# Kernel optimization log

Measured on AMD Instinct MI355X. Metric: run time of the kernel, lower is better.

Reference implementation:

```python
import jax, jax.numpy as jnp
import numpy as np

B, N, C = 16, 2048, 512
NUM_HEADS = 8
D = C // NUM_HEADS  # 64


def setup_inputs() -> dict:
    key = jax.random.key(0)
    ks = jax.random.split(key, 8)
    s = 0.02
    return {
        "x": jax.random.normal(ks[0], (B, N, C), dtype=jnp.float32),
        "Wq": jax.random.normal(ks[1], (D, C), dtype=jnp.float32) * s,
        "bq": jax.random.normal(ks[2], (D,), dtype=jnp.float32) * s,
        "Wk": jax.random.normal(ks[3], (D, C), dtype=jnp.float32) * s,
        "bk": jax.random.normal(ks[4], (D,), dtype=jnp.float32) * s,
        "Wv": jax.random.normal(ks[5], (C, C), dtype=jnp.float32) * s,
        "bv": jax.random.normal(ks[6], (C,), dtype=jnp.float32) * s,
        "gamma": jax.random.normal(ks[7], (1,), dtype=jnp.float32) * 0.1,
    }


def reference(x, Wq, bq, Wk, bk, Wv, bv, gamma):
    # x: [B, N, C]; torch code permutes to [B, C, N] (channels for Conv1d)
    xt = jnp.transpose(x, (0, 2, 1))                      # [B, C, N]
    # 1x1 Conv1d == pointwise linear over channel dim
    q = jnp.einsum('dc,bcn->bdn', Wq, xt) + bq[None, :, None]   # [B, D, N]
    k = jnp.einsum('dc,bcn->bdn', Wk, xt) + bk[None, :, None]   # [B, D, N]
    v = jnp.einsum('oc,bcn->bon', Wv, xt) + bv[None, :, None]   # [B, C, N]
    # energy[b, n, m] = <q[:, n], k[:, m]>
    energy = jnp.einsum('bdn,bdm->bnm', q, k)             # [B, N, N]
    attention = jax.nn.softmax(energy, axis=-1)           # [B, N, N]
    # out = bmm(v, attention^T): out[b, c, n] = sum_m v[b, c, m] * attn[b, n, m]
    out = jnp.einsum('bcm,bnm->bcn', v, attention)        # [B, C, N]
    out = gamma[0] * out + xt
    return jnp.transpose(out, (0, 2, 1))                  # [B, N, C]
```

## Files before the change

### kernel.cpp

```cpp
#include <hip/hip_runtime.h>
#include <hip/hip_bf16.h>

typedef __bf16 bf16x8 __attribute__((ext_vector_type(8)));
typedef float f32x4 __attribute__((ext_vector_type(4)));

#define B_ 16
#define N_ 2048
#define C_ 512
#define D_ 64

__device__ __forceinline__ float bf2f(ushort u) {
    union { uint i; float f; } w; w.i = ((uint)u) << 16; return w.f;
}
__device__ __forceinline__ ushort f2bf(float f) {
    union { float f; uint i; } w; w.f = f;
    uint u = w.i;
    u = (u + 0x7fffu + ((u >> 16) & 1u)) >> 16;
    return (ushort)u;
}
__device__ __forceinline__ __bf16 u2b(ushort u) {
    union { ushort s; __bf16 b; } w; w.s = u; return w.b;
}
__device__ __forceinline__ bf16x8 ld8u(const ushort* p) { return *(const bf16x8*)p; }
__device__ __forceinline__ bf16x8 ld8f(const float* p) {
    f32x4 a = *(const f32x4*)p;
    f32x4 b = *(const f32x4*)(p + 4);
    bf16x8 r;
    r[0] = u2b(f2bf(a[0])); r[1] = u2b(f2bf(a[1]));
    r[2] = u2b(f2bf(a[2])); r[3] = u2b(f2bf(a[3]));
    r[4] = u2b(f2bf(b[0])); r[5] = u2b(f2bf(b[1]));
    r[6] = u2b(f2bf(b[2])); r[7] = u2b(f2bf(b[3]));
    return r;
}

__device__ __forceinline__ void gload16(const ushort* g, ushort* l) {
    __builtin_amdgcn_global_load_lds(
        (const __attribute__((address_space(1))) void*)g,
        (__attribute__((address_space(3))) void*)l, 16, 0, 0);
}

__global__ void probe_kernel(const void* x, int* flag) {
    int lane = threadIdx.x & 63;
    ushort u = ((const ushort*)x)[lane * 2];
    float v = fabsf(bf2f(u));
    bool sane = (v > 9.3e-10f) && (v < 1.1e9f) && (v == v);
    unsigned long long m = __ballot(sane);
    if (threadIdx.x == 0) *flag = (__popcll(m) >= 48) ? 0 : 1;
}

__launch_bounds__(256, 2)
__global__ void proj_qk_kernel(const void* __restrict__ X,
                               const void* __restrict__ Wq_,
                               const void* __restrict__ bq_,
                               const void* __restrict__ Wk_,
                               const void* __restrict__ bk_,
                               ushort* __restrict__ outq,
                               ushort* __restrict__ outk,
                               const int* __restrict__ flag) {
    const int isf32 = *flag;
    const ushort* Xu  = (const ushort*)X;
    const float*  Xf  = (const float*)X;
    const ushort* Wqu = (const ushort*)Wq_;
    const float*  Wqf = (const float*)Wq_;
    const ushort* Wku = (const ushort*)Wk_;
    const float*  Wkf = (const float*)Wk_;
    const ushort* Bqu = (const ushort*)bq_;
    const float*  Bqf = (const float*)bq_;
    const ushort* Bku = (const ushort*)bk_;
    const float*  Bkf = (const float*)bk_;

    __shared__ ushort lA[64][72];
    __shared__ ushort lBq[64][72];
    __shared__ ushort lBk[64][72];
    const int tid  = threadIdx.x;
    const int wave = tid >> 6, lane = tid & 63;
    const int quad = lane >> 4, li = lane & 15;
    const int m0 = blockIdx.x * 64;

    f32x4 accq[4], acck[4];
    #pragma unroll
    for (int t = 0; t < 4; ++t) {
        accq[t] = (f32x4){0.f, 0.f, 0.f, 0.f};
        acck[t] = (f32x4){0.f, 0.f, 0.f, 0.f};
    }

    for (int k0 = 0; k0 < C_; k0 += 64) {
        __syncthreads();
        #pragma unroll
        for (int it = 0; it < 2; ++it) {
            int idx = tid + it * 256;
            int row = idx >> 3, seg = idx & 7;
            size_t ea = (size_t)(m0 + row) * C_ + k0 + seg * 8;
            size_t eb = (size_t)row * C_ + k0 + seg * 8;
            if (!isf32) {
                *(bf16x8*)&lA[row][seg * 8]  = ld8u(Xu + ea);
                *(bf16x8*)&lBq[row][seg * 8] = ld8u(Wqu + eb);
                *(bf16x8*)&lBk[row][seg * 8] = ld8u(Wku + eb);
            } else {
                *(bf16x8*)&lA[row][seg * 8]  = ld8f(Xf + ea);
                *(bf16x8*)&lBq[row][seg * 8] = ld8f(Wqf + eb);
                *(bf16x8*)&lBk[row][seg * 8] = ld8f(Wkf + eb);
            }
        }
        __syncthreads();
        #pragma unroll
        for (int ks = 0; ks < 2; ++ks) {
            bf16x8 a = *(const bf16x8*)&lA[wave * 16 + li][ks * 32 + quad * 8];
            #pragma unroll
            for (int t = 0; t < 4; ++t) {
                bf16x8 bq8 = *(const bf16x8*)&lBq[t * 16 + li][ks * 32 + quad * 8];
                bf16x8 bk8 = *(const bf16x8*)&lBk[t * 16 + li][ks * 32 + quad * 8];
                accq[t] = __builtin_amdgcn_mfma_f32_16x16x32_bf16(a, bq8, accq[t], 0, 0, 0);
                acck[t] = __builtin_amdgcn_mfma_f32_16x16x32_bf16(a, bk8, acck[t], 0, 0, 0);
            }
        }
    }

    #pragma unroll
    for (int t = 0; t < 4; ++t) {
        int c = t * 16 + li;
        float bvq = isf32 ? Bqf[c] : bf2f(Bqu[c]);
        float bvk = isf32 ? Bkf[c] : bf2f(Bku[c]);
        #pragma unroll
        for (int j = 0; j < 4; ++j) {
            int m = m0 + wave * 16 + quad * 4 + j;
            outq[(size_t)m * D_ + c] = f2bf(accq[t][j] + bvq);
            outk[(size_t)m * D_ + c] = f2bf(acck[t][j] + bvk);
        }
    }
}

template<int NCOLS, int MODE>
__launch_bounds__(256, 2)
__global__ void proj_kernel(const void* __restrict__ X,
                            const void* __restrict__ W,
                            const void* __restrict__ bias,
                            ushort* __restrict__ out,
                            const int* __restrict__ flag,
                            size_t xoff) {
    const int isf32 = *flag;
    const ushort* Xu = (const ushort*)X + xoff;
    const float*  Xf = (const float*)X + xoff;
    const ushort* Wu = (const ushort*)W;
    const float*  Wf = (const float*)W;
    const ushort* Bu = (const ushort*)bias;
    const float*  Bf = (const float*)bias;

    __shared__ ushort lA[64][72];
    __shared__ ushort lB[64][72];
    const int tid  = threadIdx.x;
    const int wave = tid >> 6, lane = tid & 63;
    const int quad = lane >> 4, li = lane & 15;
    const int m0 = blockIdx.x * 64;
    const int n0 = blockIdx.y * 64;

    f32x4 acc[4];
    #pragma unroll
    for (int t = 0; t < 4; ++t) acc[t] = (f32x4){0.f, 0.f, 0.f, 0.f};

    for (int k0 = 0; k0 < C_; k0 += 64) {
        __syncthreads();
        #pragma unroll
        for (int it = 0; it < 2; ++it) {
            int idx = tid + it * 256;
            int row = idx >> 3, seg = idx & 7;
            size_t ea = (size_t)(m0 + row) * C_ + k0 + seg * 8;
            size_t eb = (size_t)(n0 + row) * C_ + k0 + seg * 8;
            if (!isf32) {
                *(bf16x8*)&lA[row][seg * 8] = ld8u(Xu + ea);
                *(bf16x8*)&lB[row][seg * 8] = ld8u(Wu + eb);
            } else {
                *(bf16x8*)&lA[row][seg * 8] = ld8f(Xf + ea);
                *(bf16x8*)&lB[row][seg * 8] = ld8f(Wf + eb);
            }
        }
        __syncthreads();
        #pragma unroll
        for (int ks = 0; ks < 2; ++ks) {
            bf16x8 a = *(const bf16x8*)&lA[wave * 16 + li][ks * 32 + quad * 8];
            #pragma unroll
            for (int t = 0; t < 4; ++t) {
                bf16x8 b = *(const bf16x8*)&lB[t * 16 + li][ks * 32 + quad * 8];
                acc[t] = __builtin_amdgcn_mfma_f32_16x16x32_bf16(a, b, acc[t], 0, 0, 0);
            }
        }
    }

    #pragma unroll
    for (int t = 0; t < 4; ++t) {
        int c = n0 + t * 16 + li;
        float bv = isf32 ? Bf[c] : bf2f(Bu[c]);
        if (MODE == 0) {
            #pragma unroll
            for (int j = 0; j < 4; ++j) {
                int m = m0 + wave * 16 + quad * 4 + j;
                out[(size_t)m * NCOLS + c] = f2bf(acc[t][j] + bv);
            }
        } else {
            int m = m0 + wave * 16 + quad * 4;
            int b = m >> 11, ml = m & (N_ - 1);
            ushort4 pk;
            pk.x = f2bf(acc[t][0] + bv);
            pk.y = f2bf(acc[t][1] + bv);
            pk.z = f2bf(acc[t][2] + bv);
            pk.w = f2bf(acc[t][3] + bv);
            *(ushort4*)(out + ((size_t)(b * C_ + c)) * N_ + ml) = pk;
        }
    }
}

template<int KTOT, int SA, int SB, int EPI>
__launch_bounds__(256, 2)
__global__ void gemm128(const ushort* __restrict__ Abase,
                        const ushort* __restrict__ Bbase,
                        ushort* __restrict__ Sout,
                        float* __restrict__ lrow,
                        const void* __restrict__ x,
                        const void* __restrict__ gptr,
                        void* __restrict__ out,
                        const int* __restrict__ flag,
                        int b0, size_t aBS, size_t bBS) {
    __shared__ ushort lA[128 * 64];
    __shared__ ushort lB[128 * 64];
    const int tid  = threadIdx.x;
    const int wave = tid >> 6, lane = tid & 63;
    const int quad = lane >> 4, li = lane & 15;
    const int wr = (wave & 1) * 64;
    const int wc = (wave >> 1) * 64;
    const int bz = blockIdx.z;
    const int m0 = blockIdx.x * 128;
    const int c0 = blockIdx.y * 128;
    const ushort* A  = Abase + (size_t)bz * aBS;
    const ushort* Bp = Bbase + (size_t)bz * bBS;

    const int lrow8 = lane >> 3;
    const int lseg  = (lane & 7) ^ (lrow8 & 7);

    f32x4 acc[4][4];
    #pragma unroll
    for (int i = 0; i < 4; ++i)
        #pragma unroll
        for (int j = 0; j < 4; ++j) acc[i][j] = (f32x4){0.f, 0.f, 0.f, 0.f};

    for (int k0 = 0; k0 < KTOT; k0 += 64) {
        __syncthreads();
        #pragma unroll
        for (int i = 0; i < 4; ++i) {
            int rbase = wave * 32 + i * 8;
            int rA = m0 + rbase + lrow8;
            int rB = c0 + rbase + lrow8;
            gload16(A  + (size_t)rA * SA + k0 + lseg * 8, &lA[rbase * 64]);
            gload16(Bp + (size_t)rB * SB + k0 + lseg * 8, &lB[rbase * 64]);
        }
        __syncthreads();

        #pragma unroll
        for (int ks = 0; ks < 2; ++ks) {
            bf16x8 af[4], bfr[4];
            #pragma unroll
            for (int i = 0; i < 4; ++i) {
                int row = wr + i * 16 + li;
                af[i] = *(const bf16x8*)&lA[row * 64 + (((ks * 4 + quad) ^ (li & 7)) * 8)];
            }
            #pragma unroll
            for (int j = 0; j < 4; ++j) {
                int row = wc + j * 16 + li;
                bfr[j] = *(const bf16x8*)&lB[row * 64 + (((ks * 4 + quad) ^ (li & 7)) * 8)];
            }
            #pragma unroll
            for (int i = 0; i < 4; ++i)
                #pragma unroll
                for (int j = 0; j < 4; ++j)
                    acc[i][j] = __builtin_amdgcn_mfma_f32_16x16x32_bf16(
                        af[i], bfr[j], acc[i][j], 0, 0, 0);
        }
    }

    if (EPI == 0) {
        ushort* Sb = Sout + (size_t)bz * N_ * N_;
        float*  lb = lrow + (size_t)bz * N_;
        #pragma unroll
        for (int i = 0; i < 4; ++i)
            #pragma unroll
            for (int j = 0; j < 4; ++j) {
                int n = m0 + wr + i * 16 + quad * 4 + j;
                float s4 = 0.f;
                #pragma unroll
                for (int j2 = 0; j2 < 4; ++j2) {
                    int m = c0 + wc + j2 * 16 + li;
                    float e = __expf(fminf(acc[i][j2][j], 60.f));
                    Sb[(size_t)n * N_ + m] = f2bf(e);
                    s4 += e;
                }
                s4 += __shfl_xor(s4, 1, 64);
                s4 += __shfl_xor(s4, 2, 64);
                s4 += __shfl_xor(s4, 4, 64);
                s4 += __shfl_xor(s4, 8, 64);
                if (li == 0) atomicAdd(&lb[n], s4);
            }
    } else {
        const int isf32 = *flag;
        const ushort* xu = (const ushort*)x;
        const float*  xf = (const float*)x;
        ushort* ou = (ushort*)out;
        float*  of = (float*)out;
        float g = isf32 ? ((const float*)gptr)[0] : bf2f(((const ushort*)gptr)[0]);
        #pragma unroll
        for (int i = 0; i < 4; ++i) {
            #pragma unroll
            for (int j = 0; j < 4; ++j) {
                int n = m0 + wr + i * 16 + quad * 4 + j;
                float inv = 1.f / lrow[(size_t)bz * N_ + n];
                size_t rowb = ((size_t)((b0 + bz) * N_ + n)) * C_;
                #pragma unroll
                for (int j2 = 0; j2 < 4; ++j2) {
                    int c = c0 + wc + j2 * 16 + li;
                    size_t idx = rowb + c;
                    float xv  = isf32 ? xf[idx] : bf2f(xu[idx]);
                    float val = g * (acc[i][j2][j] * inv) + xv;
                    if (isf32) of[idx] = val; else ou[idx] = f2bf(val);
                }
            }
        }
    }
}

extern "C" void kernel_launch(void* const* d_in, const int* in_sizes, int n_in,
                              void* d_out, int out_size, void* d_ws, size_t ws_size,
                              hipStream_t stream) {
    (void)in_sizes; (void)n_in; (void)out_size;
    const void* x     = d_in[0];
    const void* Wq    = d_in[1];
    const void* bq    = d_in[2];
    const void* Wk    = d_in[3];
    const void* bk    = d_in[4];
    const void* Wv    = d_in[5];
    const void* bv    = d_in[6];
    const void* gamma = d_in[7];

    auto need = [](int bh) -> size_t {
        return 256 + 2 * (size_t)B_ * N_ * D_ * 2 +
               (size_t)bh * ((size_t)C_ * N_ * 2 + (size_t)N_ * N_ * 2 + (size_t)N_ * 4);
    };
    int BHg = 1;
    if      (need(16) <= ws_size) BHg = 16;
    else if (need(8)  <= ws_size) BHg = 8;
    else if (need(4)  <= ws_size) BHg = 4;
    else if (need(2)  <= ws_size) BHg = 2;

    int*    flag = (int*)d_ws;
    ushort* q    = (ushort*)((char*)d_ws + 256);
    ushort* kk   = q  + (size_t)B_ * N_ * D_;
    ushort* vt   = kk + (size_t)B_ * N_ * D_;
    ushort* S    = vt + (size_t)BHg * C_ * N_;
    float*  lrow = (float*)(S + (size_t)BHg * N_ * N_);

    probe_kernel<<<1, 64, 0, stream>>>(x, flag);

    const int M = B_ * N_;
    proj_qk_kernel<<<dim3(M / 64), 256, 0, stream>>>(x, Wq, bq, Wk, bk, q, kk, flag);

    for (int b0 = 0; b0 < B_; b0 += BHg) {
        const size_t xoff = (size_t)b0 * N_ * C_;
        const size_t qoff = (size_t)b0 * N_ * D_;
        proj_kernel<C_, 1><<<dim3(BHg * N_ / 64, C_ / 64), 256, 0, stream>>>(
            x, Wv, bv, vt, flag, xoff);
        hipMemsetAsync(lrow, 0, (size_t)BHg * N_ * sizeof(float), stream);
        gemm128<64, 64, 64, 0><<<dim3(16, 16, BHg), 256, 0, stream>>>(
            q + qoff, kk + qoff, S, lrow, x, gamma, d_out, flag, b0,
            (size_t)N_ * D_, (size_t)N_ * D_);
        gemm128<2048, 2048, 2048, 1><<<dim3(16, 4, BHg), 256, 0, stream>>>(
            S, vt, S, lrow, x, gamma, d_out, flag, b0,
            (size_t)N_ * N_, (size_t)C_ * N_);
    }
}
```

Measured before the change: 344.1 us.

## Fuse QK^T, exp, and PV into single flash-style attention kernel

Replaces the materialized N×N score matrix pipeline (score GEMM writing exp'd scores plus atomics for row sums, then a second GEMM reading them back) with one kernel per 64-query block that computes scores tile by tile, exponentiates into LDS, and immediately multiplies by V. This removes the large S buffer's global writes and reads, the memset, and the batch-group loop. In exchange, K and V tiles are read directly from global memory without LDS staging, each block holds 128 accumulator registers, and the grid has only 512 blocks, which may limit occupancy and memory efficiency.

```diff
diff --git a/kernel.cpp b/kernel.cpp
--- a/kernel.cpp
+++ b/kernel.cpp
@@ -31,12 +31,6 @@
     r[4] = u2b(f2bf(b[0])); r[5] = u2b(f2bf(b[1]));
     r[6] = u2b(f2bf(b[2])); r[7] = u2b(f2bf(b[3]));
     return r;
-}
-
-__device__ __forceinline__ void gload16(const ushort* g, ushort* l) {
-    __builtin_amdgcn_global_load_lds(
-        (const __attribute__((address_space(1))) void*)g,
-        (__attribute__((address_space(3))) void*)l, 16, 0, 0);
 }
 
 __global__ void probe_kernel(const void* x, int* flag) {
@@ -209,126 +203,141 @@
     }
 }
 
-template<int KTOT, int SA, int SB, int EPI>
 __launch_bounds__(256, 2)
-__global__ void gemm128(const ushort* __restrict__ Abase,
-                        const ushort* __restrict__ Bbase,
-                        ushort* __restrict__ Sout,
-                        float* __restrict__ lrow,
-                        const void* __restrict__ x,
-                        const void* __restrict__ gptr,
-                        void* __restrict__ out,
-                        const int* __restrict__ flag,
-                        int b0, size_t aBS, size_t bBS) {
-    __shared__ ushort lA[128 * 64];
-    __shared__ ushort lB[128 * 64];
+__global__ void attn_fused(const ushort* __restrict__ q,
+                           const ushort* __restrict__ kk,
+                           const ushort* __restrict__ vt,
+                           const void* __restrict__ x,
+                           const void* __restrict__ gptr,
+                           void* __restrict__ out,
+                           const int* __restrict__ flag) {
+    __shared__ ushort Pl[64 * 64];
+    __shared__ float  ll[64];
+
     const int tid  = threadIdx.x;
     const int wave = tid >> 6, lane = tid & 63;
     const int quad = lane >> 4, li = lane & 15;
-    const int wr = (wave & 1) * 64;
-    const int wc = (wave >> 1) * 64;
-    const int bz = blockIdx.z;
-    const int m0 = blockIdx.x * 128;
-    const int c0 = blockIdx.y * 128;
-    const ushort* A  = Abase + (size_t)bz * aBS;
-    const ushort* Bp = Bbase + (size_t)bz * bBS;
-
-    const int lrow8 = lane >> 3;
-    const int lseg  = (lane & 7) ^ (lrow8 & 7);
-
-    f32x4 acc[4][4];
+    const int b  = blockIdx.y;
+    const int q0 = blockIdx.x * 64;
+
+    const ushort* qrow = q + ((size_t)(b * N_ + q0 + wave * 16 + li)) * D_;
+    bf16x8 qf[2];
+    qf[0] = ld8u(qrow + quad * 8);
+    qf[1] = ld8u(qrow + 32 + quad * 8);
+
+    const ushort* kb = kk + (size_t)b * N_ * D_;
+    const ushort* vb = vt + (size_t)b * C_ * N_;
+
+    f32x4 acc[4][8];
     #pragma unroll
     for (int i = 0; i < 4; ++i)
         #pragma unroll
-        for (int j = 0; j < 4; ++j) acc[i][j] = (f32x4){0.f, 0.f, 0.f, 0.f};
-
-    for (int k0 = 0; k0 < KTOT; k0 += 64) {
-        __syncthreads();
+        for (int j = 0; j < 8; ++j) acc[i][j] = (f32x4){0.f, 0.f, 0.f, 0.f};
+
+    f32x4 accp[4];
+    #pragma unroll
+    for (int tm = 0; tm < 4; ++tm) accp[tm] = (f32x4){0.f, 0.f, 0.f, 0.f};
+    float s4[4] = {0.f, 0.f, 0.f, 0.f};
+
+    #pragma unroll
+    for (int tm = 0; tm < 4; ++tm)
+        #pragma unroll
+        for (int ks = 0; ks < 2; ++ks) {
+            bf16x8 kf = ld8u(kb + ((size_t)(tm * 16 + li)) * D_ + ks * 32 + quad * 8);
+            accp[tm] = __builtin_amdgcn_mfma_f32_16x16x32_bf16(qf[ks], kf, accp[tm], 0, 0, 0);
+        }
+
+    for (int t = 0; t < 32; ++t) {
+        __syncthreads();
+        #pragma unroll
+        for (int tm = 0; tm < 4; ++tm)
+            #pragma unroll
+            for (int j = 0; j < 4; ++j) {
+                int r = wave * 16 + quad * 4 + j;
+                int m = tm * 16 + li;
+                float e = __expf(fminf(accp[tm][j], 60.f));
+                s4[j] += e;
+                Pl[r * 64 + (((m >> 3) ^ (r & 7)) * 8) + (m & 7)] = f2bf(e);
+            }
+        __syncthreads();
+
+        if (t < 31) {
+            const int m0 = (t + 1) * 64;
+            #pragma unroll
+            for (int tm = 0; tm < 4; ++tm) accp[tm] = (f32x4){0.f, 0.f, 0.f, 0.f};
+            #pragma unroll
+            for (int tm = 0; tm < 4; ++tm)
+                #pragma unroll
+                for (int ks = 0; ks < 2; ++ks) {
+                    bf16x8 kf = ld8u(kb + ((size_t)(m0 + tm * 16 + li)) * D_ + ks * 32 + quad * 8);
+                    accp[tm] = __builtin_amdgcn_mfma_f32_16x16x32_bf16(qf[ks], kf, accp[tm], 0, 0, 0);
+                }
+        }
+
+        bf16x8 af[4][2];
         #pragma unroll
         for (int i = 0; i < 4; ++i) {
-            int rbase = wave * 32 + i * 8;
-            int rA = m0 + rbase + lrow8;
-            int rB = c0 + rbase + lrow8;
-            gload16(A  + (size_t)rA * SA + k0 + lseg * 8, &lA[rbase * 64]);
-            gload16(Bp + (size_t)rB * SB + k0 + lseg * 8, &lB[rbase * 64]);
-        }
-        __syncthreads();
-
-        #pragma unroll
-        for (int ks = 0; ks < 2; ++ks) {
-            bf16x8 af[4], bfr[4];
-            #pragma unroll
-            for (int i = 0; i < 4; ++i) {
-                int row = wr + i * 16 + li;
-                af[i] = *(const bf16x8*)&lA[row * 64 + (((ks * 4 + quad) ^ (li & 7)) * 8)];
-            }
-            #pragma unroll
-            for (int j = 0; j < 4; ++j) {
-                int row = wc + j * 16 + li;
-                bfr[j] = *(const bf16x8*)&lB[row * 64 + (((ks * 4 + quad) ^ (li & 7)) * 8)];
-            }
-            #pragma unroll
-            for (int i = 0; i < 4; ++i)
+            int row = i * 16 + li;
+            #pragma unroll
+            for (int ks = 0; ks < 2; ++ks)
+                af[i][ks] = *(const bf16x8*)&Pl[row * 64 + (((ks * 4 + quad) ^ (row & 7)) * 8)];
+        }
+        #pragma unroll
+        for (int j = 0; j < 8; ++j) {
+            int c = wave * 128 + j * 16 + li;
+            const ushort* vrow = vb + (size_t)c * N_ + t * 64;
+            #pragma unroll
+            for (int ks = 0; ks < 2; ++ks) {
+                bf16x8 vf = ld8u(vrow + ks * 32 + quad * 8);
                 #pragma unroll
-                for (int j = 0; j < 4; ++j)
+                for (int i = 0; i < 4; ++i)
                     acc[i][j] = __builtin_amdgcn_mfma_f32_16x16x32_bf16(
-                        af[i], bfr[j], acc[i][j], 0, 0, 0);
-        }
-    }
-
-    if (EPI == 0) {
-        ushort* Sb = Sout + (size_t)bz * N_ * N_;
-        float*  lb = lrow + (size_t)bz * N_;
-        #pragma unroll
-        for (int i = 0; i < 4; ++i)
-            #pragma unroll
-            for (int j = 0; j < 4; ++j) {
-                int n = m0 + wr + i * 16 + quad * 4 + j;
-                float s4 = 0.f;
-                #pragma unroll
-                for (int j2 = 0; j2 < 4; ++j2) {
-                    int m = c0 + wc + j2 * 16 + li;
-                    float e = __expf(fminf(acc[i][j2][j], 60.f));
-                    Sb[(size_t)n * N_ + m] = f2bf(e);
-                    s4 += e;
-                }
-                s4 += __shfl_xor(s4, 1, 64);
-                s4 += __shfl_xor(s4, 2, 64);
-                s4 += __shfl_xor(s4, 4, 64);
-                s4 += __shfl_xor(s4, 8, 64);
-                if (li == 0) atomicAdd(&lb[n], s4);
-            }
-    } else {
-        const int isf32 = *flag;
-        const ushort* xu = (const ushort*)x;
-        const float*  xf = (const float*)x;
-        ushort* ou = (ushort*)out;
-        float*  of = (float*)out;
-        float g = isf32 ? ((const float*)gptr)[0] : bf2f(((const ushort*)gptr)[0]);
-        #pragma unroll
-        for (int i = 0; i < 4; ++i) {
-            #pragma unroll
-            for (int j = 0; j < 4; ++j) {
-                int n = m0 + wr + i * 16 + quad * 4 + j;
-                float inv = 1.f / lrow[(size_t)bz * N_ + n];
-                size_t rowb = ((size_t)((b0 + bz) * N_ + n)) * C_;
-                #pragma unroll
-                for (int j2 = 0; j2 < 4; ++j2) {
-                    int c = c0 + wc + j2 * 16 + li;
-                    size_t idx = rowb + c;
-                    float xv  = isf32 ? xf[idx] : bf2f(xu[idx]);
-                    float val = g * (acc[i][j2][j] * inv) + xv;
-                    if (isf32) of[idx] = val; else ou[idx] = f2bf(val);
-                }
-            }
-        }
-    }
+                        af[i][ks], vf, acc[i][j], 0, 0, 0);
+            }
+        }
+    }
+
+    #pragma unroll
+    for (int j = 0; j < 4; ++j) {
+        s4[j] += __shfl_xor(s4[j], 1, 64);
+        s4[j] += __shfl_xor(s4[j], 2, 64);
+        s4[j] += __shfl_xor(s4[j], 4, 64);
+        s4[j] += __shfl_xor(s4[j], 8, 64);
+    }
+    if (li == 0) {
+        #pragma unroll
+        for (int j = 0; j < 4; ++j) ll[wave * 16 + quad * 4 + j] = s4[j];
+    }
+    __syncthreads();
+
+    const int isf32 = *flag;
+    const float g = isf32 ? ((const float*)gptr)[0] : bf2f(((const ushort*)gptr)[0]);
+    const ushort* xu = (const ushort*)x;
+    const float*  xf = (const float*)x;
+    ushort* ou = (ushort*)out;
+    float*  of = (float*)out;
+    #pragma unroll
+    for (int i = 0; i < 4; ++i)
+        #pragma unroll
+        for (int jj = 0; jj < 4; ++jj) {
+            int nl = i * 16 + quad * 4 + jj;
+            float inv = 1.f / ll[nl];
+            size_t rowb = ((size_t)(b * N_ + q0 + nl)) * C_;
+            #pragma unroll
+            for (int j = 0; j < 8; ++j) {
+                int c = wave * 128 + j * 16 + li;
+                size_t idx = rowb + c;
+                float xv  = isf32 ? xf[idx] : bf2f(xu[idx]);
+                float val = g * (acc[i][j][jj] * inv) + xv;
+                if (isf32) of[idx] = val; else ou[idx] = f2bf(val);
+            }
+        }
 }
 
 extern "C" void kernel_launch(void* const* d_in, const int* in_sizes, int n_in,
                               void* d_out, int out_size, void* d_ws, size_t ws_size,
                               hipStream_t stream) {
-    (void)in_sizes; (void)n_in; (void)out_size;
+    (void)in_sizes; (void)n_in; (void)out_size; (void)ws_size;
     const void* x     = d_in[0];
     const void* Wq    = d_in[1];
     const void* bq    = d_in[2];
@@ -338,39 +347,17 @@
     const void* bv    = d_in[6];
     const void* gamma = d_in[7];
 
-    auto need = [](int bh) -> size_t {
-        return 256 + 2 * (size_t)B_ * N_ * D_ * 2 +
-               (size_t)bh * ((size_t)C_ * N_ * 2 + (size_t)N_ * N_ * 2 + (size_t)N_ * 4);
-    };
-    int BHg = 1;
-    if      (need(16) <= ws_size) BHg = 16;
-    else if (need(8)  <= ws_size) BHg = 8;
-    else if (need(4)  <= ws_size) BHg = 4;
-    else if (need(2)  <= ws_size) BHg = 2;
-
     int*    flag = (int*)d_ws;
     ushort* q    = (ushort*)((char*)d_ws + 256);
     ushort* kk   = q  + (size_t)B_ * N_ * D_;
     ushort* vt   = kk + (size_t)B_ * N_ * D_;
-    ushort* S    = vt + (size_t)BHg * C_ * N_;
-    float*  lrow = (float*)(S + (size_t)BHg * N_ * N_);
 
     probe_kernel<<<1, 64, 0, stream>>>(x, flag);
 
     const int M = B_ * N_;
     proj_qk_kernel<<<dim3(M / 64), 256, 0, stream>>>(x, Wq, bq, Wk, bk, q, kk, flag);
-
-    for (int b0 = 0; b0 < B_; b0 += BHg) {
-        const size_t xoff = (size_t)b0 * N_ * C_;
-        const size_t qoff = (size_t)b0 * N_ * D_;
-        proj_kernel<C_, 1><<<dim3(BHg * N_ / 64, C_ / 64), 256, 0, stream>>>(
-            x, Wv, bv, vt, flag, xoff);
-        hipMemsetAsync(lrow, 0, (size_t)BHg * N_ * sizeof(float), stream);
-        gemm128<64, 64, 64, 0><<<dim3(16, 16, BHg), 256, 0, stream>>>(
-            q + qoff, kk + qoff, S, lrow, x, gamma, d_out, flag, b0,
-            (size_t)N_ * D_, (size_t)N_ * D_);
-        gemm128<2048, 2048, 2048, 1><<<dim3(16, 4, BHg), 256, 0, stream>>>(
-            S, vt, S, lrow, x, gamma, d_out, flag, b0,
-            (size_t)N_ * N_, (size_t)C_ * N_);
-    }
-}
+    proj_kernel<C_, 1><<<dim3(M / 64, C_ / 64), 256, 0, stream>>>(
+        x, Wv, bv, vt, flag, 0);
+    attn_fused<<<dim3(N_ / 64, B_), 256, 0, stream>>>(
+        q, kk, vt, x, gamma, d_out, flag);
+}
```

Measured after the change: 447.7 us. +30.1%, slower.
